# Optimization experiments

Measured on AMD Instinct MI355X. Metric: run time of the kernel, lower is better.

The kernel has to match this reference:

```python
import jax, jax.numpy as jnp
import numpy as np

U = 100001          # user_count = user_num + 1
I = 50001           # item_count = item_num + 1
N = U + I           # total nodes
D = 64              # embedding dim
E = 3_200_000       # user-item interactions
NNZ = 2 * E         # symmetric directed edges
N_LAYERS = 3


def setup_inputs() -> dict:
    key = jax.random.key(0)
    k1, k2, k3, k4 = jax.random.split(key, 4)
    user_emb = jax.random.normal(k1, (U, D), dtype=jnp.float32) * 0.1
    item_emb = jax.random.normal(k2, (I, D), dtype=jnp.float32) * 0.1
    # random bipartite interactions, symmetrized like _get_a_adj_matrix
    u = jax.random.randint(k3, (E,), 0, U, dtype=jnp.int32)
    it = jax.random.randint(k4, (E,), 0, I, dtype=jnp.int32)
    rows = jnp.concatenate([u, it + U])            # [NNZ]
    cols = jnp.concatenate([it + U, u])            # [NNZ]
    # D^{-1/2} A D^{-1/2}: deg from row sums of A (values are 1s, duplicates sum)
    deg = jax.ops.segment_sum(jnp.ones((NNZ,), jnp.float32), rows, num_segments=N) + 1e-7
    dinv = deg ** -0.5
    vals = dinv[rows] * dinv[cols]                 # [NNZ]
    return {"user_emb": user_emb, "item_emb": item_emb,
            "rows": rows, "cols": cols, "vals": vals}


def _spmm(rows, cols, vals, x):
    # out[r] += vals * x[c]  (COO SpMM via gather + segment_sum)
    return jax.ops.segment_sum(vals[:, None] * x[cols], rows, num_segments=N)


def reference(user_emb, item_emb, rows, cols, vals):
    all_emb = jnp.concatenate([user_emb, item_emb], axis=0)   # [N, D]
    acc = all_emb                                             # running sum over layers (== mean * (L+1))
    h = all_emb
    for _ in range(N_LAYERS):
        h = _spmm(rows, cols, vals, h)
        acc = acc + h
    out = acc / (N_LAYERS + 1)                                # mean over stacked layers
    return out[:U], out[U:]
```

## Files before the change

### kernel.cpp

```cpp
#include <hip/hip_runtime.h>
#include <hip/hip_fp16.h>

#define U_CNT 100001
#define I_CNT 50001
#define N_CNT 150002
#define DIM 64
#define BROWS 512
#define NB2 ((N_CNT + BROWS - 1) / BROWS)
#define NB2P 512
#define CH 8192

__device__ inline __half2 u2h(unsigned int u) { union { unsigned int u; __half2 h; } c; c.u = u; return c.h; }
__device__ inline unsigned int h2u(__half2 h) { union { unsigned int u; __half2 h; } c; c.h = h; return c.u; }

__global__ void bucket_hist(const int* __restrict__ rows, int* __restrict__ bhist,
                            int nnz) {
    __shared__ int lh[NB2];
    for (int i = threadIdx.x; i < NB2; i += blockDim.x) lh[i] = 0;
    __syncthreads();
    int stride = gridDim.x * blockDim.x;
    for (int i = blockIdx.x * blockDim.x + threadIdx.x; i < nnz; i += stride)
        atomicAdd(&lh[rows[i] >> 9], 1);
    __syncthreads();
    for (int i = threadIdx.x; i < NB2; i += blockDim.x) {
        int v = lh[i];
        if (v) atomicAdd(&bhist[i], v);
    }
}

__global__ void bucket_scan(const int* __restrict__ bhist,
                            int* __restrict__ bucket_ptr,
                            int* __restrict__ bcur) {
    if (threadIdx.x == 0 && blockIdx.x == 0) {
        int run = 0;
        for (int i = 0; i < NB2; ++i) {
            bucket_ptr[i] = run;
            bcur[i] = run;
            run += bhist[i];
        }
        bucket_ptr[NB2] = run;
    }
}

__global__ void __launch_bounds__(256) partition_kernel(
    const int* __restrict__ rows, const int* __restrict__ cols,
    int* __restrict__ bcur, unsigned int* __restrict__ staging, int nnz)
{
    __shared__ int hist[NB2P];
    __shared__ int ofs[NB2 + 1];
    __shared__ int cur[NB2];
    __shared__ int gbase[NB2];
    __shared__ unsigned int recs[CH];
    const int t = threadIdx.x;
    int base = blockIdx.x * CH;
    int lim = nnz - base; if (lim > CH) lim = CH;

    for (int i = t; i < NB2P; i += 256) hist[i] = 0;
    __syncthreads();
    for (int i = t; i < lim; i += 256)
        atomicAdd(&hist[rows[base + i] >> 9], 1);
    __syncthreads();
    for (int off = 1; off < NB2P; off <<= 1) {
        int v0 = (t >= off) ? hist[t - off] : 0;
        int i1 = t + 256;
        int v1 = hist[i1 - off];
        __syncthreads();
        hist[t] += v0;
        hist[i1] += v1;
        __syncthreads();
    }
    for (int i = t; i <= NB2; i += 256)
        ofs[i] = (i == 0) ? 0 : hist[i - 1];
    __syncthreads();
    for (int i = t; i < NB2; i += 256)
        cur[i] = ofs[i];
    __syncthreads();
    for (int i = t; i < NB2; i += 256) {
        int cnt = ofs[i + 1] - ofs[i];
        if (cnt) gbase[i] = atomicAdd(&bcur[i], cnt);
    }
    for (int i = t; i < lim; i += 256) {
        int r = rows[base + i];
        int c = cols[base + i];
        int p = atomicAdd(&cur[r >> 9], 1);
        recs[p] = ((unsigned int)c << 9) | (unsigned int)(r & (BROWS - 1));
    }
    __syncthreads();
    for (int p = t; p < lim; p += 256) {
        unsigned int rec = recs[p];
        int lo = 0, hi = NB2;
        while (hi - lo > 1) {
            int mid = (lo + hi) >> 1;
            if (ofs[mid] <= p) lo = mid; else hi = mid;
        }
        staging[gbase[lo] + (p - ofs[lo])] = rec;
    }
}

__global__ void binplace_kernel(const int* __restrict__ bucket_ptr,
                                const unsigned int* __restrict__ staging,
                                unsigned int* __restrict__ col_s,
                                int* __restrict__ row_ptr,
                                float* __restrict__ dinv) {
    __shared__ int hist[BROWS];
    __shared__ int cur[BROWS];
    int b = blockIdx.x;
    int base = b << 9;
    int beg = bucket_ptr[b];
    int end = bucket_ptr[b + 1];
    int t = threadIdx.x;
    hist[t] = 0;
    __syncthreads();
    for (int j = beg + t; j < end; j += BROWS)
        atomicAdd(&hist[staging[j] & (BROWS - 1u)], 1);
    __syncthreads();
    int cnt = hist[t];
    for (int off = 1; off < BROWS; off <<= 1) {
        int v = (t >= off) ? hist[t - off] : 0;
        __syncthreads();
        hist[t] += v;
        __syncthreads();
    }
    int start = beg + hist[t] - cnt;
    cur[t] = start;
    int r = base + t;
    if (r < N_CNT) {
        row_ptr[r] = start;
        dinv[r] = 1.0f / sqrtf((float)cnt + 1e-7f);
    }
    if (b == NB2 - 1 && t == 0) row_ptr[N_CNT] = end;
    __syncthreads();
    for (int j = beg + t; j < end; j += BROWS) {
        unsigned int rec = staging[j];
        int pos = atomicAdd(&cur[rec & (BROWS - 1u)], 1);
        col_s[pos] = rec >> 9;
    }
}

__global__ void init_kernel(const float4* __restrict__ ue,
                            const float4* __restrict__ ie,
                            const float* __restrict__ dinv,
                            uint4* __restrict__ hs,
                            float4* __restrict__ acc) {
    int i = blockIdx.x * blockDim.x + threadIdx.x;
    if (i >= N_CNT * 8) return;
    int node = i >> 3;
    int s = i & 7;
    float d = dinv[node];
    size_t fo = (size_t)node * 16 + s * 2;
    float4 v0, v1;
    if (node < U_CNT) { v0 = ue[fo]; v1 = ue[fo + 1]; }
    else { size_t io = fo - (size_t)U_CNT * 16; v0 = ie[io]; v1 = ie[io + 1]; }
    acc[fo] = v0;
    acc[fo + 1] = v1;
    uint4 h;
    h.x = h2u(__floats2half2_rn(d * v0.x, d * v0.y));
    h.y = h2u(__floats2half2_rn(d * v0.z, d * v0.w));
    h.z = h2u(__floats2half2_rn(d * v1.x, d * v1.y));
    h.w = h2u(__floats2half2_rn(d * v1.z, d * v1.w));
    hs[(size_t)node * 8 + s] = h;
}

__device__ inline void acc8(float4& a0, float4& a1, uint4 u) {
    float2 f;
    f = __half22float2(u2h(u.x)); a0.x += f.x; a0.y += f.y;
    f = __half22float2(u2h(u.y)); a0.z += f.x; a0.w += f.y;
    f = __half22float2(u2h(u.z)); a1.x += f.x; a1.y += f.y;
    f = __half22float2(u2h(u.w)); a1.z += f.x; a1.w += f.y;
}

__global__ void spmm_gather(const int* __restrict__ row_ptr,
                            const unsigned int* __restrict__ col_s,
                            const float* __restrict__ dinv,
                            const uint4* __restrict__ x,
                            uint4* __restrict__ y,
                            float4* __restrict__ acc,
                            int r0, int r1, int last) {
    int r = r0 + blockIdx.x * 32 + (threadIdx.x >> 3);
    int s = threadIdx.x & 7;
    if (r >= r1) return;
    int beg = row_ptr[r];
    int end = row_ptr[r + 1];
    float4 a0 = {0.f, 0.f, 0.f, 0.f}, a1 = {0.f, 0.f, 0.f, 0.f};
    float4 b0 = {0.f, 0.f, 0.f, 0.f}, b1 = {0.f, 0.f, 0.f, 0.f};
    int j = beg;
    for (; j + 4 <= end; j += 4) {
        unsigned int c0 = col_s[j];
        unsigned int c1 = col_s[j + 1];
        unsigned int c2 = col_s[j + 2];
        unsigned int c3 = col_s[j + 3];
        uint4 u0 = x[(size_t)c0 * 8 + s];
        uint4 u1 = x[(size_t)c1 * 8 + s];
        uint4 u2 = x[(size_t)c2 * 8 + s];
        uint4 u3 = x[(size_t)c3 * 8 + s];
        acc8(a0, a1, u0);
        acc8(b0, b1, u1);
        acc8(a0, a1, u2);
        acc8(b0, b1, u3);
    }
    for (; j < end; ++j) {
        unsigned int c0 = col_s[j];
        uint4 u0 = x[(size_t)c0 * 8 + s];
        acc8(a0, a1, u0);
    }
    a0.x += b0.x; a0.y += b0.y; a0.z += b0.z; a0.w += b0.w;
    a1.x += b1.x; a1.y += b1.y; a1.z += b1.z; a1.w += b1.w;

    float d = dinv[r];
    float d2 = d * d;
    uint4 h;
    h.x = h2u(__floats2half2_rn(d2 * a0.x, d2 * a0.y));
    h.y = h2u(__floats2half2_rn(d2 * a0.z, d2 * a0.w));
    h.z = h2u(__floats2half2_rn(d2 * a1.x, d2 * a1.y));
    h.w = h2u(__floats2half2_rn(d2 * a1.z, d2 * a1.w));
    y[(size_t)r * 8 + s] = h;

    size_t o = (size_t)r * 16 + s * 2;
    float4 c0 = acc[o];
    float4 c1 = acc[o + 1];
    c0.x += d * a0.x; c0.y += d * a0.y; c0.z += d * a0.z; c0.w += d * a0.w;
    c1.x += d * a1.x; c1.y += d * a1.y; c1.z += d * a1.z; c1.w += d * a1.w;
    if (last) {
        c0.x *= 0.25f; c0.y *= 0.25f; c0.z *= 0.25f; c0.w *= 0.25f;
        c1.x *= 0.25f; c1.y *= 0.25f; c1.z *= 0.25f; c1.w *= 0.25f;
    }
    acc[o] = c0;
    acc[o + 1] = c1;
}

extern "C" void kernel_launch(void* const* d_in, const int* in_sizes, int n_in,
                              void* d_out, int out_size, void* d_ws, size_t ws_size,
                              hipStream_t stream) {
    const float* ue   = (const float*)d_in[0];
    const float* ie   = (const float*)d_in[1];
    const int*   rows = (const int*)d_in[2];
    const int*   cols = (const int*)d_in[3];
    int nnz = in_sizes[2];

    float* acc = (float*)d_out;

    unsigned int* ws = (unsigned int*)d_ws;
    uint4* hs0 = (uint4*)ws;
    uint4* hs1 = hs0 + (size_t)N_CNT * 8;
    int*   row_ptr    = (int*)(hs1 + (size_t)N_CNT * 8);
    int*   bhist      = row_ptr + (N_CNT + 1);
    int*   bucket_ptr = bhist + NB2;
    int*   bcur       = bucket_ptr + (NB2 + 1);
    float* dinv       = (float*)(bcur + NB2);
    unsigned int* staging = (unsigned int*)(dinv + N_CNT);
    unsigned int* col_s   = staging + nnz;

    const int tpb = 256;

    hipMemsetAsync(bhist, 0, NB2 * sizeof(int), stream);
    bucket_hist<<<512, tpb, 0, stream>>>(rows, bhist, nnz);
    bucket_scan<<<1, 64, 0, stream>>>(bhist, bucket_ptr, bcur);
    partition_kernel<<<(nnz + CH - 1) / CH, tpb, 0, stream>>>(
        rows, cols, bcur, staging, nnz);
    binplace_kernel<<<NB2, BROWS, 0, stream>>>(
        bucket_ptr, staging, col_s, row_ptr, dinv);

    init_kernel<<<(N_CNT * 8 + tpb - 1) / tpb, tpb, 0, stream>>>(
        (const float4*)ue, (const float4*)ie, dinv, hs0, (float4*)acc);

    uint4* cur = hs0;
    uint4* nxt = hs1;
    const int ublocks = (U_CNT + 31) / 32;
    const int iblocks = (N_CNT - U_CNT + 31) / 32;
    for (int l = 0; l < 3; ++l) {
        int last = (l == 2) ? 1 : 0;
        spmm_gather<<<ublocks, tpb, 0, stream>>>(
            row_ptr, col_s, dinv, cur, nxt, (float4*)acc, 0, U_CNT, last);
        spmm_gather<<<iblocks, tpb, 0, stream>>>(
            row_ptr, col_s, dinv, cur, nxt, (float4*)acc, U_CNT, N_CNT, last);
        uint4* tmp = cur; cur = nxt; nxt = tmp;
    }
}
```

Before: 633.4 us.

## Split SpMM by feature halves, shrink row buckets, parallelize scans, stage binplace in LDS

The SpMM now processes each 32-wide half of the fp16 embedding in a separate launch, with 4 threads per row. This narrows the gathered working set per sweep so it stays cache-resident, at the cost of extra launches and rereading row_ptr and col_s twice. Preprocessing uses 128-row buckets and replaces the single-thread bucket scan with a parallel block scan. binplace sorts records into an LDS window before writing col_s, so the global writes are coalesced.

```diff
diff --git a/kernel.cpp b/kernel.cpp
--- a/kernel.cpp
+++ b/kernel.cpp
@@ -5,10 +5,10 @@
 #define I_CNT 50001
 #define N_CNT 150002
 #define DIM 64
-#define BROWS 512
+#define BROWS 128
 #define NB2 ((N_CNT + BROWS - 1) / BROWS)
-#define NB2P 512
 #define CH 8192
+#define WCAP 12288
 
 __device__ inline __half2 u2h(unsigned int u) { union { unsigned int u; __half2 h; } c; c.u = u; return c.h; }
 __device__ inline unsigned int h2u(__half2 h) { union { unsigned int u; __half2 h; } c; c.h = h; return c.u; }
@@ -20,7 +20,7 @@
     __syncthreads();
     int stride = gridDim.x * blockDim.x;
     for (int i = blockIdx.x * blockDim.x + threadIdx.x; i < nnz; i += stride)
-        atomicAdd(&lh[rows[i] >> 9], 1);
+        atomicAdd(&lh[rows[i] >> 7], 1);
     __syncthreads();
     for (int i = threadIdx.x; i < NB2; i += blockDim.x) {
         int v = lh[i];
@@ -31,59 +31,77 @@
 __global__ void bucket_scan(const int* __restrict__ bhist,
                             int* __restrict__ bucket_ptr,
                             int* __restrict__ bcur) {
-    if (threadIdx.x == 0 && blockIdx.x == 0) {
-        int run = 0;
-        for (int i = 0; i < NB2; ++i) {
-            bucket_ptr[i] = run;
-            bcur[i] = run;
-            run += bhist[i];
-        }
-        bucket_ptr[NB2] = run;
-    }
+    __shared__ int lds[1024];
+    int t = threadIdx.x;
+    int b0 = t * 2;
+    int b1 = b0 + 2; if (b1 > NB2) b1 = NB2;
+    int s = 0;
+    for (int i = b0; i < b1 && i < NB2; ++i) s += bhist[i];
+    lds[t] = s;
+    __syncthreads();
+    for (int off = 1; off < 1024; off <<= 1) {
+        int v = (t >= off) ? lds[t - off] : 0;
+        __syncthreads();
+        lds[t] += v;
+        __syncthreads();
+    }
+    int run = (t == 0) ? 0 : lds[t - 1];
+    for (int i = b0; i < b1 && i < NB2; ++i) {
+        bucket_ptr[i] = run;
+        bcur[i] = run;
+        run += bhist[i];
+    }
+    if (t == 1023) bucket_ptr[NB2] = lds[1023];
 }
 
 __global__ void __launch_bounds__(256) partition_kernel(
     const int* __restrict__ rows, const int* __restrict__ cols,
     int* __restrict__ bcur, unsigned int* __restrict__ staging, int nnz)
 {
-    __shared__ int hist[NB2P];
+    __shared__ int hist[NB2];
     __shared__ int ofs[NB2 + 1];
     __shared__ int cur[NB2];
     __shared__ int gbase[NB2];
+    __shared__ int tsum[256];
     __shared__ unsigned int recs[CH];
     const int t = threadIdx.x;
     int base = blockIdx.x * CH;
     int lim = nnz - base; if (lim > CH) lim = CH;
 
-    for (int i = t; i < NB2P; i += 256) hist[i] = 0;
+    for (int i = t; i < NB2; i += 256) hist[i] = 0;
     __syncthreads();
     for (int i = t; i < lim; i += 256)
-        atomicAdd(&hist[rows[base + i] >> 9], 1);
-    __syncthreads();
-    for (int off = 1; off < NB2P; off <<= 1) {
-        int v0 = (t >= off) ? hist[t - off] : 0;
-        int i1 = t + 256;
-        int v1 = hist[i1 - off];
-        __syncthreads();
-        hist[t] += v0;
-        hist[i1] += v1;
-        __syncthreads();
-    }
-    for (int i = t; i <= NB2; i += 256)
-        ofs[i] = (i == 0) ? 0 : hist[i - 1];
-    __syncthreads();
-    for (int i = t; i < NB2; i += 256)
-        cur[i] = ofs[i];
+        atomicAdd(&hist[rows[base + i] >> 7], 1);
+    __syncthreads();
+    int b0 = t * 5;
+    int b1 = b0 + 5; if (b1 > NB2) b1 = NB2;
+    int s = 0;
+    for (int i = b0; i < b1; ++i) s += hist[i];
+    tsum[t] = s;
+    __syncthreads();
+    for (int off = 1; off < 256; off <<= 1) {
+        int v = (t >= off) ? tsum[t - off] : 0;
+        __syncthreads();
+        tsum[t] += v;
+        __syncthreads();
+    }
+    int run = (t == 0) ? 0 : tsum[t - 1];
+    for (int i = b0; i < b1; ++i) {
+        ofs[i] = run;
+        cur[i] = run;
+        run += hist[i];
+    }
+    if (t == 0) ofs[NB2] = lim;
     __syncthreads();
     for (int i = t; i < NB2; i += 256) {
-        int cnt = ofs[i + 1] - ofs[i];
+        int cnt = hist[i];
         if (cnt) gbase[i] = atomicAdd(&bcur[i], cnt);
     }
     for (int i = t; i < lim; i += 256) {
         int r = rows[base + i];
         int c = cols[base + i];
-        int p = atomicAdd(&cur[r >> 9], 1);
-        recs[p] = ((unsigned int)c << 9) | (unsigned int)(r & (BROWS - 1));
+        int p = atomicAdd(&cur[r >> 7], 1);
+        recs[p] = ((unsigned int)c << 7) | (unsigned int)(r & (BROWS - 1));
     }
     __syncthreads();
     for (int p = t; p < lim; p += 256) {
@@ -97,43 +115,60 @@
     }
 }
 
-__global__ void binplace_kernel(const int* __restrict__ bucket_ptr,
-                                const unsigned int* __restrict__ staging,
-                                unsigned int* __restrict__ col_s,
-                                int* __restrict__ row_ptr,
-                                float* __restrict__ dinv) {
+__global__ void __launch_bounds__(256) binplace_kernel(
+    const int* __restrict__ bucket_ptr,
+    const unsigned int* __restrict__ staging,
+    unsigned int* __restrict__ col_s,
+    int* __restrict__ row_ptr,
+    float* __restrict__ dinv)
+{
     __shared__ int hist[BROWS];
     __shared__ int cur[BROWS];
+    __shared__ unsigned int win[WCAP];
     int b = blockIdx.x;
-    int base = b << 9;
+    int base = b << 7;
     int beg = bucket_ptr[b];
     int end = bucket_ptr[b + 1];
+    int tot = end - beg;
     int t = threadIdx.x;
-    hist[t] = 0;
-    __syncthreads();
-    for (int j = beg + t; j < end; j += BROWS)
+    if (t < BROWS) hist[t] = 0;
+    __syncthreads();
+    for (int j = beg + t; j < end; j += 256)
         atomicAdd(&hist[staging[j] & (BROWS - 1u)], 1);
     __syncthreads();
-    int cnt = hist[t];
+    int cnt = (t < BROWS) ? hist[t] : 0;
     for (int off = 1; off < BROWS; off <<= 1) {
-        int v = (t >= off) ? hist[t - off] : 0;
-        __syncthreads();
-        hist[t] += v;
-        __syncthreads();
-    }
-    int start = beg + hist[t] - cnt;
-    cur[t] = start;
-    int r = base + t;
-    if (r < N_CNT) {
-        row_ptr[r] = start;
-        dinv[r] = 1.0f / sqrtf((float)cnt + 1e-7f);
+        int v = (t < BROWS && t >= off) ? hist[t - off] : 0;
+        __syncthreads();
+        if (t < BROWS) hist[t] += v;
+        __syncthreads();
+    }
+    if (t < BROWS) {
+        int excl = hist[t] - cnt;
+        cur[t] = excl;
+        int r = base + t;
+        if (r < N_CNT) {
+            row_ptr[r] = beg + excl;
+            dinv[r] = 1.0f / sqrtf((float)cnt + 1e-7f);
+        }
     }
     if (b == NB2 - 1 && t == 0) row_ptr[N_CNT] = end;
     __syncthreads();
-    for (int j = beg + t; j < end; j += BROWS) {
-        unsigned int rec = staging[j];
-        int pos = atomicAdd(&cur[rec & (BROWS - 1u)], 1);
-        col_s[pos] = rec >> 9;
+    if (tot <= WCAP) {
+        for (int j = beg + t; j < end; j += 256) {
+            unsigned int rec = staging[j];
+            int pos = atomicAdd(&cur[rec & (BROWS - 1u)], 1);
+            win[pos] = rec >> 7;
+        }
+        __syncthreads();
+        for (int p = t; p < tot; p += 256)
+            col_s[beg + p] = win[p];
+    } else {
+        for (int j = beg + t; j < end; j += 256) {
+            unsigned int rec = staging[j];
+            int pos = atomicAdd(&cur[rec & (BROWS - 1u)], 1);
+            col_s[beg + pos] = rec >> 7;
+        }
     }
 }
 
@@ -169,18 +204,21 @@
     f = __half22float2(u2h(u.w)); a1.z += f.x; a1.w += f.y;
 }
 
-__global__ void spmm_gather(const int* __restrict__ row_ptr,
-                            const unsigned int* __restrict__ col_s,
-                            const float* __restrict__ dinv,
-                            const uint4* __restrict__ x,
-                            uint4* __restrict__ y,
-                            float4* __restrict__ acc,
-                            int r0, int r1, int last) {
-    int r = r0 + blockIdx.x * 32 + (threadIdx.x >> 3);
-    int s = threadIdx.x & 7;
+__global__ void __launch_bounds__(256) spmm_gather(
+    const int* __restrict__ row_ptr,
+    const unsigned int* __restrict__ col_s,
+    const float* __restrict__ dinv,
+    const uint4* __restrict__ x,
+    uint4* __restrict__ y,
+    float4* __restrict__ acc,
+    int r0, int r1, int halfsel, int last)
+{
+    int r = r0 + blockIdx.x * 64 + (threadIdx.x >> 2);
+    int s = threadIdx.x & 3;
     if (r >= r1) return;
     int beg = row_ptr[r];
     int end = row_ptr[r + 1];
+    int hb = (halfsel << 2) + s;
     float4 a0 = {0.f, 0.f, 0.f, 0.f}, a1 = {0.f, 0.f, 0.f, 0.f};
     float4 b0 = {0.f, 0.f, 0.f, 0.f}, b1 = {0.f, 0.f, 0.f, 0.f};
     int j = beg;
@@ -189,10 +227,10 @@
         unsigned int c1 = col_s[j + 1];
         unsigned int c2 = col_s[j + 2];
         unsigned int c3 = col_s[j + 3];
-        uint4 u0 = x[(size_t)c0 * 8 + s];
-        uint4 u1 = x[(size_t)c1 * 8 + s];
-        uint4 u2 = x[(size_t)c2 * 8 + s];
-        uint4 u3 = x[(size_t)c3 * 8 + s];
+        uint4 u0 = x[(size_t)c0 * 8 + hb];
+        uint4 u1 = x[(size_t)c1 * 8 + hb];
+        uint4 u2 = x[(size_t)c2 * 8 + hb];
+        uint4 u3 = x[(size_t)c3 * 8 + hb];
         acc8(a0, a1, u0);
         acc8(b0, b1, u1);
         acc8(a0, a1, u2);
@@ -200,7 +238,7 @@
     }
     for (; j < end; ++j) {
         unsigned int c0 = col_s[j];
-        uint4 u0 = x[(size_t)c0 * 8 + s];
+        uint4 u0 = x[(size_t)c0 * 8 + hb];
         acc8(a0, a1, u0);
     }
     a0.x += b0.x; a0.y += b0.y; a0.z += b0.z; a0.w += b0.w;
@@ -213,9 +251,9 @@
     h.y = h2u(__floats2half2_rn(d2 * a0.z, d2 * a0.w));
     h.z = h2u(__floats2half2_rn(d2 * a1.x, d2 * a1.y));
     h.w = h2u(__floats2half2_rn(d2 * a1.z, d2 * a1.w));
-    y[(size_t)r * 8 + s] = h;
-
-    size_t o = (size_t)r * 16 + s * 2;
+    y[(size_t)r * 8 + hb] = h;
+
+    size_t o = (size_t)r * 16 + (halfsel << 3) + s * 2;
     float4 c0 = acc[o];
     float4 c1 = acc[o + 1];
     c0.x += d * a0.x; c0.y += d * a0.y; c0.z += d * a0.z; c0.w += d * a0.w;
@@ -254,10 +292,10 @@
 
     hipMemsetAsync(bhist, 0, NB2 * sizeof(int), stream);
     bucket_hist<<<512, tpb, 0, stream>>>(rows, bhist, nnz);
-    bucket_scan<<<1, 64, 0, stream>>>(bhist, bucket_ptr, bcur);
+    bucket_scan<<<1, 1024, 0, stream>>>(bhist, bucket_ptr, bcur);
     partition_kernel<<<(nnz + CH - 1) / CH, tpb, 0, stream>>>(
         rows, cols, bcur, staging, nnz);
-    binplace_kernel<<<NB2, BROWS, 0, stream>>>(
+    binplace_kernel<<<NB2, tpb, 0, stream>>>(
         bucket_ptr, staging, col_s, row_ptr, dinv);
 
     init_kernel<<<(N_CNT * 8 + tpb - 1) / tpb, tpb, 0, stream>>>(
@@ -265,14 +303,18 @@
 
     uint4* cur = hs0;
     uint4* nxt = hs1;
-    const int ublocks = (U_CNT + 31) / 32;
-    const int iblocks = (N_CNT - U_CNT + 31) / 32;
+    const int ublocks = (U_CNT + 63) / 64;
+    const int iblocks = (I_CNT + 63) / 64;
     for (int l = 0; l < 3; ++l) {
         int last = (l == 2) ? 1 : 0;
         spmm_gather<<<ublocks, tpb, 0, stream>>>(
-            row_ptr, col_s, dinv, cur, nxt, (float4*)acc, 0, U_CNT, last);
+            row_ptr, col_s, dinv, cur, nxt, (float4*)acc, 0, U_CNT, 0, last);
+        spmm_gather<<<ublocks, tpb, 0, stream>>>(
+            row_ptr, col_s, dinv, cur, nxt, (float4*)acc, 0, U_CNT, 1, last);
         spmm_gather<<<iblocks, tpb, 0, stream>>>(
-            row_ptr, col_s, dinv, cur, nxt, (float4*)acc, U_CNT, N_CNT, last);
+            row_ptr, col_s, dinv, cur, nxt, (float4*)acc, U_CNT, N_CNT, 0, last);
+        spmm_gather<<<iblocks, tpb, 0, stream>>>(
+            row_ptr, col_s, dinv, cur, nxt, (float4*)acc, U_CNT, N_CNT, 1, last);
         uint4* tmp = cur; cur = nxt; nxt = tmp;
     }
 }
```

After: 959.8 us. 51.5% more time.
